# Kernel optimization log

Hardware: AMD Instinct MI355X
Metric: run time of the kernel (lower is better)

## Reference

```python
import jax, jax.numpy as jnp
import numpy as np

N_NODES = 100000
N_EDGES = 1600000
IN_FEATS = 256
OUT_FEATS = 128


def setup_inputs() -> dict:
    key = jax.random.key(0)
    k1, k2, k3, k4 = jax.random.split(key, 4)
    feat = jax.random.normal(k1, (N_NODES, IN_FEATS), dtype=jnp.float32)
    # Glorot-uniform-like weight
    limit = np.sqrt(6.0 / (IN_FEATS + OUT_FEATS)).astype(np.float32)
    weight = jax.random.uniform(k2, (IN_FEATS, OUT_FEATS), dtype=jnp.float32,
                                minval=-limit, maxval=limit)
    bias = jnp.zeros((OUT_FEATS,), dtype=jnp.float32)
    src = jax.random.randint(k3, (N_EDGES,), 0, N_NODES, dtype=jnp.int32)
    dst = jax.random.randint(k4, (N_EDGES,), 0, N_NODES, dtype=jnp.int32)
    return {"feat": feat, "weight": weight, "bias": bias, "src": src, "dst": dst}


def reference(feat, weight, bias, src, dst):
    n = feat.shape[0]
    # in-degree per node (edges point src -> dst), clipped to >= 1
    deg = jax.ops.segment_sum(jnp.ones_like(dst, dtype=feat.dtype), dst,
                              num_segments=n)
    norm = jnp.clip(deg, 1.0, None) ** -0.5          # [N]
    norm = norm[:, None]                             # [N, 1]
    h = feat * norm                                  # src-side normalization
    # in_feats > out_feats: project first, then aggregate (cheaper messages)
    h = h @ weight                                   # [N, out]
    agg = jax.ops.segment_sum(h[src], dst, num_segments=n)  # sparse sum-aggregate
    rst = agg * norm + bias                          # dst-side norm + bias
    return rst
```

## Files before the change

kernel.cpp:

```cpp
#include <hip/hip_runtime.h>

#define IN_F 256
#define OUT_F 128
#define BSH 7
#define BNODES 128
#define MAXBUCK 1024
#define BIN1A_BLOCKS 256
#define BIN1B_BLOCKS 256

typedef short bf16x8 __attribute__((ext_vector_type(8)));
typedef float f32x4 __attribute__((ext_vector_type(4)));
typedef unsigned short us8 __attribute__((ext_vector_type(8)));

__device__ inline unsigned short f2bf(float x) {
    union { float f; unsigned u; } v; v.f = x;
    unsigned r = v.u + 0x7FFFu + ((v.u >> 16) & 1u);
    return (unsigned short)(r >> 16);
}
__device__ inline float bf2f(unsigned short x) {
    union { unsigned u; float f; } v; v.u = ((unsigned)x) << 16;
    return v.f;
}

__global__ __launch_bounds__(256) void prep_kernel(const float* __restrict__ W,
                                                   unsigned short* __restrict__ Wt,
                                                   const int* __restrict__ dst,
                                                   int* __restrict__ bhist,
                                                   int n_edges, int nbuck) {
    if ((int)blockIdx.x < BIN1A_BLOCKS) {
        __shared__ int hist[MAXBUCK];
        const int tid = threadIdx.x;
        const int chunk = (n_edges + BIN1A_BLOCKS - 1) / BIN1A_BLOCKS;
        const int lo = blockIdx.x * chunk;
        const int hi = min(lo + chunk, n_edges);

        for (int i = tid; i < MAXBUCK; i += 256) hist[i] = 0;
        __syncthreads();
        for (int e = lo + tid; e < hi; e += 256)
            atomicAdd(&hist[dst[e] >> BSH], 1);
        __syncthreads();
        for (int i = tid; i < nbuck; i += 256) {
            int c = hist[i];
            if (c) atomicAdd(&bhist[i], c);
        }
    } else {
        int n = blockIdx.x - BIN1A_BLOCKS;
        int k = threadIdx.x;
        Wt[n * IN_F + k] = f2bf(W[k * OUT_F + n]);
    }
}

__global__ __launch_bounds__(1024) void gemm_bin_kernel(
        const float* __restrict__ feat, const unsigned short* __restrict__ Wt,
        unsigned short* __restrict__ h, int n_nodes,
        const int* __restrict__ src, const int* __restrict__ dst,
        const int* __restrict__ bhist, int* __restrict__ gcur0,
        unsigned* __restrict__ ebuf, int n_edges, int nbuck) {

    __shared__ __align__(16) char smem[65536];

    if ((int)blockIdx.x < BIN1B_BLOCKS) {
        int* scanv = (int*)smem;
        int* hist  = scanv + MAXBUCK;
        int* lbase = hist + MAXBUCK;
        const int tid = threadIdx.x;
        const int chunk = (n_edges + BIN1B_BLOCKS - 1) / BIN1B_BLOCKS;
        const int lo = blockIdx.x * chunk;
        const int hi = min(lo + chunk, n_edges);

        int own = (tid < nbuck) ? bhist[tid] : 0;
        scanv[tid] = own;
        __syncthreads();
        #pragma unroll
        for (int off = 1; off < MAXBUCK; off <<= 1) {
            int t = (tid >= off) ? scanv[tid - off] : 0;
            __syncthreads();
            scanv[tid] += t;
            __syncthreads();
        }
        int bstart_t = scanv[tid] - own;
        __syncthreads();
        scanv[tid] = bstart_t;
        hist[tid] = 0;
        __syncthreads();

        for (int e = lo + tid; e < hi; e += 1024)
            atomicAdd(&hist[dst[e] >> BSH], 1);
        __syncthreads();
        if (tid < nbuck) {
            int c = hist[tid];
            lbase[tid] = (c > 0) ? (scanv[tid] + atomicAdd(&gcur0[tid], c)) : 0;
            hist[tid] = 0;
        }
        __syncthreads();
        for (int e = lo + tid; e < hi; e += 1024) {
            int d = dst[e];
            int bkt = d >> BSH;
            int off = atomicAdd(&hist[bkt], 1);
            ebuf[lbase[bkt] + off] = ((unsigned)src[e] << BSH) | (unsigned)(d & (BNODES - 1));
        }
    } else {
        unsigned short* Bs = (unsigned short*)smem;

        const int tid  = threadIdx.x;
        const int wave = tid >> 6;
        const int lane = tid & 63;
        const int gb   = blockIdx.x - BIN1B_BLOCKS;
        const int r0   = (gb * 16 + wave) * 16;
        const int lrow = lane & 15;
        const int g    = lane >> 4;
        const int kgrp = g * 8;

        {
            const f32x4* srcv = reinterpret_cast<const f32x4*>(Wt);
            f32x4* dstv = reinterpret_cast<f32x4*>(Bs);
            #pragma unroll
            for (int i = 0; i < 4; ++i) {
                int c   = tid + i * 1024;
                int row = c >> 5;
                int col = c & 31;
                dstv[c] = srcv[row * 32 + (col ^ (row & 7))];
            }
        }

        const int row  = r0 + lrow;
        const int rowc = (row < n_nodes) ? row : (n_nodes - 1);
        const float* arow = feat + (size_t)rowc * IN_F;

        __syncthreads();

        f32x4 acc[8];
        #pragma unroll
        for (int n = 0; n < 8; ++n) acc[n] = (f32x4){0.f, 0.f, 0.f, 0.f};

        const bf16x8* bsv = reinterpret_cast<const bf16x8*>(Bs);

        #pragma unroll
        for (int k0 = 0; k0 < IN_F / 32; ++k0) {
            const f32x4 a0 = *reinterpret_cast<const f32x4*>(arow + k0 * 32 + kgrp);
            const f32x4 a1 = *reinterpret_cast<const f32x4*>(arow + k0 * 32 + kgrp + 4);
            bf16x8 afr;
            afr[0] = (short)f2bf(a0[0]);
            afr[1] = (short)f2bf(a0[1]);
            afr[2] = (short)f2bf(a0[2]);
            afr[3] = (short)f2bf(a0[3]);
            afr[4] = (short)f2bf(a1[0]);
            afr[5] = (short)f2bf(a1[1]);
            afr[6] = (short)f2bf(a1[2]);
            afr[7] = (short)f2bf(a1[3]);
            #pragma unroll
            for (int n = 0; n < 8; ++n) {
                const int brow = n * 16 + lrow;
                bf16x8 bfr = bsv[brow * 32 + ((k0 * 4 + g) ^ (brow & 7))];
                acc[n] = __builtin_amdgcn_mfma_f32_16x16x32_bf16(afr, bfr, acc[n], 0, 0, 0);
            }
        }

        const int orow0 = r0 + g * 4;
        #pragma unroll
        for (int n = 0; n < 8; ++n) {
            #pragma unroll
            for (int j = 0; j < 4; ++j) {
                int orow = orow0 + j;
                if (orow < n_nodes)
                    h[(size_t)orow * OUT_F + n * 16 + lrow] = f2bf(acc[n][j]);
            }
        }
    }
}

__global__ __launch_bounds__(256) void bin2_kernel(const unsigned* __restrict__ ebuf,
                                                   const int* __restrict__ bhist,
                                                   int* __restrict__ rstart,
                                                   float* __restrict__ norm,
                                                   int* __restrict__ eidx,
                                                   int n_nodes, int nbuck) {
    __shared__ int bs[MAXBUCK];
    __shared__ int lcnt[BNODES];
    __shared__ int lex[BNODES];
    const int tid = threadIdx.x;
    const int node0 = blockIdx.x << BSH;

    {
        int v[4], s = 0;
        #pragma unroll
        for (int j = 0; j < 4; ++j) {
            int idx = tid * 4 + j;
            v[j] = (idx < nbuck) ? bhist[idx] : 0;
            s += v[j];
        }
        lexinit:;
        __shared__ int sh[256];
        sh[tid] = s;
        __syncthreads();
        #pragma unroll
        for (int off = 1; off < 256; off <<= 1) {
            int t = (tid >= off) ? sh[tid - off] : 0;
            __syncthreads();
            sh[tid] += t;
            __syncthreads();
        }
        int ex = sh[tid] - s;
        #pragma unroll
        for (int j = 0; j < 4; ++j) {
            bs[tid * 4 + j] = ex;
            ex += v[j];
        }
    }
    __syncthreads();

    const int e0 = bs[blockIdx.x];
    const int e1 = e0 + bhist[blockIdx.x];

    if (tid < BNODES) lcnt[tid] = 0;
    __syncthreads();
    for (int e = e0 + tid; e < e1; e += 256)
        atomicAdd(&lcnt[ebuf[e] & (BNODES - 1)], 1);
    __syncthreads();

    int own = (tid < BNODES) ? lcnt[tid] : 0;
    if (tid < BNODES) lex[tid] = own;
    __syncthreads();
    #pragma unroll
    for (int off = 1; off < BNODES; off <<= 1) {
        int t = (tid >= off && tid < BNODES) ? lex[tid - off] : 0;
        __syncthreads();
        if (tid < BNODES) lex[tid] += t;
        __syncthreads();
    }
    if (tid < BNODES) {
        int ex = lex[tid] - own;
        lex[tid] = ex;
        int g = node0 + tid;
        if (g <= n_nodes) rstart[g] = e0 + ex;
        if (g < n_nodes) {
            float d = (float)own;
            if (d < 1.0f) d = 1.0f;
            norm[g] = 1.0f / sqrtf(d);
        }
        lcnt[tid] = 0;
    }
    __syncthreads();

    for (int e = e0 + tid; e < e1; e += 256) {
        unsigned pk = ebuf[e];
        int dl = pk & (BNODES - 1);
        int pos = atomicAdd(&lcnt[dl], 1);
        eidx[e0 + lex[dl] + pos] = (int)(pk >> BSH);
    }
}

__global__ __launch_bounds__(256) void agg_kernel(const unsigned short* __restrict__ h,
                                                  const int* __restrict__ eidx,
                                                  const int* __restrict__ rstart,
                                                  const float* __restrict__ norm,
                                                  const float* __restrict__ bias,
                                                  float* __restrict__ out,
                                                  int n_nodes) {
    const int wave = threadIdx.x >> 6;
    const int lane = threadIdx.x & 63;
    const int grp  = lane >> 4;
    const int gl   = lane & 15;
    const int node = blockIdx.x * 4 + wave;
    if (node >= n_nodes) return;

    const int start = rstart[node];
    const int cnt   = rstart[node + 1] - start;
    const unsigned short* __restrict__ hb = h + gl * 8;

    float acc[8] = {0.f, 0.f, 0.f, 0.f, 0.f, 0.f, 0.f, 0.f};

    for (int base = 0; base < cnt; base += 64) {
        const int rem = min(64, cnt - base);
        int   ev = (lane < rem) ? eidx[start + base + lane] : 0;
        float nv = (lane < rem) ? norm[ev] : 0.f;

        int j = 0;
        for (; j + 16 <= rem; j += 16) {
            int   s0 = __shfl(ev, j + grp);
            int   s1 = __shfl(ev, j + grp + 4);
            int   s2 = __shfl(ev, j + grp + 8);
            int   s3 = __shfl(ev, j + grp + 12);
            float n0 = __shfl(nv, j + grp);
            float n1 = __shfl(nv, j + grp + 4);
            float n2 = __shfl(nv, j + grp + 8);
            float n3 = __shfl(nv, j + grp + 12);
            us8 v0 = *reinterpret_cast<const us8*>(hb + (size_t)s0 * OUT_F);
            us8 v1 = *reinterpret_cast<const us8*>(hb + (size_t)s1 * OUT_F);
            us8 v2 = *reinterpret_cast<const us8*>(hb + (size_t)s2 * OUT_F);
            us8 v3 = *reinterpret_cast<const us8*>(hb + (size_t)s3 * OUT_F);
            #pragma unroll
            for (int q = 0; q < 8; ++q) {
                acc[q] += bf2f(v0[q]) * n0 + bf2f(v1[q]) * n1
                        + bf2f(v2[q]) * n2 + bf2f(v3[q]) * n3;
            }
        }
        for (; j < rem; j += 4) {
            int   je = j + grp;
            int   jc = min(je, rem - 1);
            int   s  = __shfl(ev, jc);
            float nm = __shfl(nv, jc);
            if (je >= rem) nm = 0.f;
            us8 v = *reinterpret_cast<const us8*>(hb + (size_t)s * OUT_F);
            #pragma unroll
            for (int q = 0; q < 8; ++q)
                acc[q] += bf2f(v[q]) * nm;
        }
    }

    #pragma unroll
    for (int q = 0; q < 8; ++q) {
        acc[q] += __shfl_xor(acc[q], 16);
        acc[q] += __shfl_xor(acc[q], 32);
    }

    if (grp == 0) {
        const float nd = norm[node];
        const float4 b0 = *reinterpret_cast<const float4*>(bias + gl * 8);
        const float4 b1 = *reinterpret_cast<const float4*>(bias + gl * 8 + 4);
        float4 r0, r1;
        r0.x = acc[0] * nd + b0.x;
        r0.y = acc[1] * nd + b0.y;
        r0.z = acc[2] * nd + b0.z;
        r0.w = acc[3] * nd + b0.w;
        r1.x = acc[4] * nd + b1.x;
        r1.y = acc[5] * nd + b1.y;
        r1.z = acc[6] * nd + b1.z;
        r1.w = acc[7] * nd + b1.w;
        float* o = out + (size_t)node * OUT_F + gl * 8;
        *reinterpret_cast<float4*>(o)     = r0;
        *reinterpret_cast<float4*>(o + 4) = r1;
    }
}

extern "C" void kernel_launch(void* const* d_in, const int* in_sizes, int n_in,
                              void* d_out, int out_size, void* d_ws, size_t ws_size,
                              hipStream_t stream) {
    const float* feat   = (const float*)d_in[0];
    const float* weight = (const float*)d_in[1];
    const float* bias   = (const float*)d_in[2];
    const int*   src    = (const int*)d_in[3];
    const int*   dst    = (const int*)d_in[4];
    float* out = (float*)d_out;

    const int n_nodes = in_sizes[0] / IN_F;
    const int n_edges = in_sizes[3];
    const int nbuck   = (n_nodes + BNODES - 1) >> BSH;
    const int gemm_blocks = (n_nodes + 255) / 256;

    char* ws = (char*)d_ws;
    size_t off = 0;
    auto alloc = [&](size_t bytes) {
        char* p = ws + off;
        off += (bytes + 15) & ~(size_t)15;
        return p;
    };
    unsigned short* h  = (unsigned short*)alloc((size_t)n_nodes * OUT_F * 2);
    float* norm        = (float*)alloc((size_t)n_nodes * 4);
    int*   rstart      = (int*)alloc(((size_t)n_nodes + 1) * 4);
    int*   bhist       = (int*)alloc(2 * MAXBUCK * 4);
    int*   gcur0       = bhist + MAXBUCK;
    unsigned short* Wt = (unsigned short*)alloc((size_t)OUT_F * IN_F * 2);
    unsigned* ebuf     = (unsigned*)alloc((size_t)n_edges * 4);
    int*   eidx        = (int*)alloc((size_t)n_edges * 4);

    hipMemsetAsync(bhist, 0, 2 * MAXBUCK * sizeof(int), stream);
    prep_kernel<<<BIN1A_BLOCKS + OUT_F, 256, 0, stream>>>(weight, Wt, dst, bhist,
                                                          n_edges, nbuck);
    gemm_bin_kernel<<<BIN1B_BLOCKS + gemm_blocks, 1024, 0, stream>>>(
        feat, Wt, h, n_nodes, src, dst, bhist, gcur0, ebuf, n_edges, nbuck);
    bin2_kernel<<<nbuck, 256, 0, stream>>>(ebuf, bhist, rstart, norm, eidx,
                                           n_nodes, nbuck);
    agg_kernel<<<(n_nodes + 3) / 4, 256, 0, stream>>>(h, eidx, rstart, norm, bias, out, n_nodes);
}
```

Baseline: 146.3 us.

## Split fused GEMM/binning kernel and use persistent double-buffered LDS-DMA GEMM

Splits the combined GEMM plus edge-binning kernel into two separate kernels. The GEMM becomes a persistent 256-block kernel that stages W once per block and double-buffers 32-row feature tiles into LDS with global_load_lds (swizzled), overlapping each next tile's load with the MFMA work on the current one. The goal is to stop reloading W per block and to hide feature-load latency. In exchange, the GEMM and binning phases no longer run concurrently, and each block uses a large LDS footprint (about 128 KB), which limits occupancy.

```diff
diff --git a/kernel.cpp b/kernel.cpp
--- a/kernel.cpp
+++ b/kernel.cpp
@@ -7,6 +7,8 @@
 #define MAXBUCK 1024
 #define BIN1A_BLOCKS 256
 #define BIN1B_BLOCKS 256
+#define GEMM_BLOCKS 256
+#define BM 32
 
 typedef short bf16x8 __attribute__((ext_vector_type(8)));
 typedef float f32x4 __attribute__((ext_vector_type(4)));
@@ -20,6 +22,13 @@
 __device__ inline float bf2f(unsigned short x) {
     union { unsigned u; float f; } v; v.u = ((unsigned)x) << 16;
     return v.f;
+}
+
+__device__ __forceinline__ void gload_lds16(const void* g, void* l) {
+    __builtin_amdgcn_global_load_lds(
+        (const __attribute__((address_space(1))) unsigned int*)g,
+        (__attribute__((address_space(3))) unsigned int*)l,
+        16, 0, 0);
 }
 
 __global__ __launch_bounds__(256) void prep_kernel(const float* __restrict__ W,
@@ -50,95 +59,118 @@
     }
 }
 
-__global__ __launch_bounds__(1024) void gemm_bin_kernel(
-        const float* __restrict__ feat, const unsigned short* __restrict__ Wt,
-        unsigned short* __restrict__ h, int n_nodes,
-        const int* __restrict__ src, const int* __restrict__ dst,
-        const int* __restrict__ bhist, int* __restrict__ gcur0,
-        unsigned* __restrict__ ebuf, int n_edges, int nbuck) {
-
-    __shared__ __align__(16) char smem[65536];
-
-    if ((int)blockIdx.x < BIN1B_BLOCKS) {
-        int* scanv = (int*)smem;
-        int* hist  = scanv + MAXBUCK;
-        int* lbase = hist + MAXBUCK;
-        const int tid = threadIdx.x;
-        const int chunk = (n_edges + BIN1B_BLOCKS - 1) / BIN1B_BLOCKS;
-        const int lo = blockIdx.x * chunk;
-        const int hi = min(lo + chunk, n_edges);
-
-        int own = (tid < nbuck) ? bhist[tid] : 0;
-        scanv[tid] = own;
-        __syncthreads();
-        #pragma unroll
-        for (int off = 1; off < MAXBUCK; off <<= 1) {
-            int t = (tid >= off) ? scanv[tid - off] : 0;
-            __syncthreads();
-            scanv[tid] += t;
-            __syncthreads();
-        }
-        int bstart_t = scanv[tid] - own;
-        __syncthreads();
-        scanv[tid] = bstart_t;
+__global__ __launch_bounds__(1024) void bin1b_kernel(const int* __restrict__ src,
+                                                     const int* __restrict__ dst,
+                                                     const int* __restrict__ bhist,
+                                                     int* __restrict__ gcur0,
+                                                     unsigned* __restrict__ ebuf,
+                                                     int n_edges, int nbuck) {
+    __shared__ int scanv[MAXBUCK];
+    __shared__ int hist[MAXBUCK];
+    __shared__ int lbase[MAXBUCK];
+    const int tid = threadIdx.x;
+    const int chunk = (n_edges + BIN1B_BLOCKS - 1) / BIN1B_BLOCKS;
+    const int lo = blockIdx.x * chunk;
+    const int hi = min(lo + chunk, n_edges);
+
+    int own = (tid < nbuck) ? bhist[tid] : 0;
+    scanv[tid] = own;
+    __syncthreads();
+    #pragma unroll
+    for (int off = 1; off < MAXBUCK; off <<= 1) {
+        int t = (tid >= off) ? scanv[tid - off] : 0;
+        __syncthreads();
+        scanv[tid] += t;
+        __syncthreads();
+    }
+    int bstart_t = scanv[tid] - own;
+    __syncthreads();
+    scanv[tid] = bstart_t;
+    hist[tid] = 0;
+    __syncthreads();
+
+    for (int e = lo + tid; e < hi; e += 1024)
+        atomicAdd(&hist[dst[e] >> BSH], 1);
+    __syncthreads();
+    if (tid < nbuck) {
+        int c = hist[tid];
+        lbase[tid] = (c > 0) ? (scanv[tid] + atomicAdd(&gcur0[tid], c)) : 0;
         hist[tid] = 0;
-        __syncthreads();
-
-        for (int e = lo + tid; e < hi; e += 1024)
-            atomicAdd(&hist[dst[e] >> BSH], 1);
-        __syncthreads();
-        if (tid < nbuck) {
-            int c = hist[tid];
-            lbase[tid] = (c > 0) ? (scanv[tid] + atomicAdd(&gcur0[tid], c)) : 0;
-            hist[tid] = 0;
-        }
-        __syncthreads();
-        for (int e = lo + tid; e < hi; e += 1024) {
-            int d = dst[e];
-            int bkt = d >> BSH;
-            int off = atomicAdd(&hist[bkt], 1);
-            ebuf[lbase[bkt] + off] = ((unsigned)src[e] << BSH) | (unsigned)(d & (BNODES - 1));
-        }
-    } else {
-        unsigned short* Bs = (unsigned short*)smem;
-
-        const int tid  = threadIdx.x;
-        const int wave = tid >> 6;
-        const int lane = tid & 63;
-        const int gb   = blockIdx.x - BIN1B_BLOCKS;
-        const int r0   = (gb * 16 + wave) * 16;
-        const int lrow = lane & 15;
-        const int g    = lane >> 4;
-        const int kgrp = g * 8;
-
-        {
-            const f32x4* srcv = reinterpret_cast<const f32x4*>(Wt);
-            f32x4* dstv = reinterpret_cast<f32x4*>(Bs);
+    }
+    __syncthreads();
+    for (int e = lo + tid; e < hi; e += 1024) {
+        int d = dst[e];
+        int bkt = d >> BSH;
+        int off = atomicAdd(&hist[bkt], 1);
+        ebuf[lbase[bkt] + off] = ((unsigned)src[e] << BSH) | (unsigned)(d & (BNODES - 1));
+    }
+}
+
+__global__ __launch_bounds__(256) void gemm_mfma(const float* __restrict__ feat,
+                                                 const unsigned short* __restrict__ Wt,
+                                                 unsigned short* __restrict__ h,
+                                                 int n_nodes) {
+    __shared__ float As[2][BM * IN_F];
+    __shared__ unsigned short Bs[OUT_F * IN_F];
+
+    const int tid  = threadIdx.x;
+    const int wave = tid >> 6;
+    const int lane = tid & 63;
+    const int q    = lane >> 4;
+    const int rr   = lane & 15;
+    const int rowgrp = wave & 1;
+    const int nhalf  = wave >> 1;
+
+    const int ntiles = (n_nodes + BM - 1) / BM;
+
+    #pragma unroll
+    for (int m = 0; m < 16; ++m) {
+        int p   = m * 4 + wave;
+        int row = 2 * p + (lane >> 5);
+        int ch  = lane & 31;
+        gload_lds16(Wt + (size_t)row * IN_F + ((ch ^ (row & 7)) * 8),
+                    &Bs[p * 2 * IN_F]);
+    }
+
+    int t = blockIdx.x;
+    if (t < ntiles) {
+        const int R0 = t * BM;
+        #pragma unroll
+        for (int i = 0; i < 8; ++i) {
+            int r  = i * 4 + wave;
+            int rg = R0 + r; if (rg >= n_nodes) rg = n_nodes - 1;
+            gload_lds16(feat + (size_t)rg * IN_F + ((lane ^ (r & 7)) * 4),
+                        &As[0][r * IN_F]);
+        }
+    }
+    __syncthreads();
+
+    int buf = 0;
+    for (; t < ntiles; t += GEMM_BLOCKS) {
+        const int tn = t + GEMM_BLOCKS;
+        if (tn < ntiles) {
+            const int R0n = tn * BM;
             #pragma unroll
-            for (int i = 0; i < 4; ++i) {
-                int c   = tid + i * 1024;
-                int row = c >> 5;
-                int col = c & 31;
-                dstv[c] = srcv[row * 32 + (col ^ (row & 7))];
+            for (int i = 0; i < 8; ++i) {
+                int r  = i * 4 + wave;
+                int rg = R0n + r; if (rg >= n_nodes) rg = n_nodes - 1;
+                gload_lds16(feat + (size_t)rg * IN_F + ((lane ^ (r & 7)) * 4),
+                            &As[buf ^ 1][r * IN_F]);
             }
         }
 
-        const int row  = r0 + lrow;
-        const int rowc = (row < n_nodes) ? row : (n_nodes - 1);
-        const float* arow = feat + (size_t)rowc * IN_F;
-
-        __syncthreads();
-
-        f32x4 acc[8];
-        #pragma unroll
-        for (int n = 0; n < 8; ++n) acc[n] = (f32x4){0.f, 0.f, 0.f, 0.f};
-
+        f32x4 acc[4];
+        #pragma unroll
+        for (int n = 0; n < 4; ++n) acc[n] = (f32x4){0.f, 0.f, 0.f, 0.f};
+
+        const int arow = rowgrp * 16 + rr;
+        const f32x4* ap = reinterpret_cast<const f32x4*>(&As[buf][arow * IN_F]);
         const bf16x8* bsv = reinterpret_cast<const bf16x8*>(Bs);
 
         #pragma unroll
-        for (int k0 = 0; k0 < IN_F / 32; ++k0) {
-            const f32x4 a0 = *reinterpret_cast<const f32x4*>(arow + k0 * 32 + kgrp);
-            const f32x4 a1 = *reinterpret_cast<const f32x4*>(arow + k0 * 32 + kgrp + 4);
+        for (int k0 = 0; k0 < 8; ++k0) {
+            f32x4 a0 = ap[(k0 * 8 + 2 * q)     ^ (rr & 7)];
+            f32x4 a1 = ap[(k0 * 8 + 2 * q + 1) ^ (rr & 7)];
             bf16x8 afr;
             afr[0] = (short)f2bf(a0[0]);
             afr[1] = (short)f2bf(a0[1]);
@@ -149,23 +181,27 @@
             afr[6] = (short)f2bf(a1[2]);
             afr[7] = (short)f2bf(a1[3]);
             #pragma unroll
-            for (int n = 0; n < 8; ++n) {
-                const int brow = n * 16 + lrow;
-                bf16x8 bfr = bsv[brow * 32 + ((k0 * 4 + g) ^ (brow & 7))];
+            for (int n = 0; n < 4; ++n) {
+                const int brow = (nhalf * 4 + n) * 16 + rr;
+                bf16x8 bfr = bsv[brow * 32 + ((k0 * 4 + q) ^ (brow & 7))];
                 acc[n] = __builtin_amdgcn_mfma_f32_16x16x32_bf16(afr, bfr, acc[n], 0, 0, 0);
             }
         }
 
-        const int orow0 = r0 + g * 4;
-        #pragma unroll
-        for (int n = 0; n < 8; ++n) {
+        __syncthreads();
+
+        const int orow0 = t * BM + rowgrp * 16 + q * 4;
+        #pragma unroll
+        for (int n = 0; n < 4; ++n) {
+            const int col = (nhalf * 4 + n) * 16 + rr;
             #pragma unroll
             for (int j = 0; j < 4; ++j) {
                 int orow = orow0 + j;
                 if (orow < n_nodes)
-                    h[(size_t)orow * OUT_F + n * 16 + lrow] = f2bf(acc[n][j]);
+                    h[(size_t)orow * OUT_F + col] = f2bf(acc[n][j]);
             }
         }
+        buf ^= 1;
     }
 }
 
@@ -178,6 +214,7 @@
     __shared__ int bs[MAXBUCK];
     __shared__ int lcnt[BNODES];
     __shared__ int lex[BNODES];
+    __shared__ int sh[256];
     const int tid = threadIdx.x;
     const int node0 = blockIdx.x << BSH;
 
@@ -189,8 +226,6 @@
             v[j] = (idx < nbuck) ? bhist[idx] : 0;
             s += v[j];
         }
-        lexinit:;
-        __shared__ int sh[256];
         sh[tid] = s;
         __syncthreads();
         #pragma unroll
@@ -290,9 +325,9 @@
             us8 v2 = *reinterpret_cast<const us8*>(hb + (size_t)s2 * OUT_F);
             us8 v3 = *reinterpret_cast<const us8*>(hb + (size_t)s3 * OUT_F);
             #pragma unroll
-            for (int q = 0; q < 8; ++q) {
-                acc[q] += bf2f(v0[q]) * n0 + bf2f(v1[q]) * n1
-                        + bf2f(v2[q]) * n2 + bf2f(v3[q]) * n3;
+            for (int qq = 0; qq < 8; ++qq) {
+                acc[qq] += bf2f(v0[qq]) * n0 + bf2f(v1[qq]) * n1
+                         + bf2f(v2[qq]) * n2 + bf2f(v3[qq]) * n3;
             }
         }
         for (; j < rem; j += 4) {
@@ -303,15 +338,15 @@
             if (je >= rem) nm = 0.f;
             us8 v = *reinterpret_cast<const us8*>(hb + (size_t)s * OUT_F);
             #pragma unroll
-            for (int q = 0; q < 8; ++q)
-                acc[q] += bf2f(v[q]) * nm;
+            for (int qq = 0; qq < 8; ++qq)
+                acc[qq] += bf2f(v[qq]) * nm;
         }
     }
 
     #pragma unroll
-    for (int q = 0; q < 8; ++q) {
-        acc[q] += __shfl_xor(acc[q], 16);
-        acc[q] += __shfl_xor(acc[q], 32);
+    for (int qq = 0; qq < 8; ++qq) {
+        acc[qq] += __shfl_xor(acc[qq], 16);
+        acc[qq] += __shfl_xor(acc[qq], 32);
     }
 
     if (grp == 0) {
@@ -346,7 +381,6 @@
     const int n_nodes = in_sizes[0] / IN_F;
     const int n_edges = in_sizes[3];
     const int nbuck   = (n_nodes + BNODES - 1) >> BSH;
-    const int gemm_blocks = (n_nodes + 255) / 256;
 
     char* ws = (char*)d_ws;
     size_t off = 0;
@@ -367,8 +401,9 @@
     hipMemsetAsync(bhist, 0, 2 * MAXBUCK * sizeof(int), stream);
     prep_kernel<<<BIN1A_BLOCKS + OUT_F, 256, 0, stream>>>(weight, Wt, dst, bhist,
                                                           n_edges, nbuck);
-    gemm_bin_kernel<<<BIN1B_BLOCKS + gemm_blocks, 1024, 0, stream>>>(
-        feat, Wt, h, n_nodes, src, dst, bhist, gcur0, ebuf, n_edges, nbuck);
+    gemm_mfma<<<GEMM_BLOCKS, 256, 0, stream>>>(feat, Wt, h, n_nodes);
+    bin1b_kernel<<<BIN1B_BLOCKS, 1024, 0, stream>>>(src, dst, bhist, gcur0,
+                                                    ebuf, n_edges, nbuck);
     bin2_kernel<<<nbuck, 256, 0, stream>>>(ebuf, bhist, rstart, norm, eidx,
                                            n_nodes, nbuck);
     agg_kernel<<<(n_nodes + 3) / 4, 256, 0, stream>>>(h, eidx, rstart, norm, bias, out, n_nodes);
```

Result: slower. 154.6 us (+5.7%).
